# Kernel optimization log

Hardware: AMD Instinct MI355X
Metric: run time of the kernel (lower is better)

The kernel has to match this reference:

```python
import jax, jax.numpy as jnp
import numpy as np

B, V, K, D, E, NE = 32, 512, 16, 128, 32, 8192


def setup_inputs() -> dict:
    key = jax.random.key(0)
    ks = jax.random.split(key, 12)
    s = 0.05
    return {
        "vertex_features": jax.random.normal(ks[0], (B, V, D), jnp.float32),
        "atom_adj": jax.random.randint(ks[1], (B * V * K,), 0, B * V),
        "bond_adj": jax.random.randint(ks[2], (B * V * K,), 0, B * NE),
        "h0": jax.random.normal(ks[3], (B, V, D), jnp.float32),
        "lamda": jnp.full((1,), 0.5, jnp.float32),
        "alpha": jnp.full((1,), 0.1, jnp.float32),
        "l": 1,
        "edge_initial": jax.random.normal(ks[4], (B, NE, E), jnp.float32),
        "vertex_mask": jnp.ones((B, V), jnp.float32),
        "nbs_mask": jax.random.uniform(ks[5], (B, V, K), jnp.float32),
        # label_U1: (D+E) -> D ; label_U2: 2D -> D ; feature_updating: D -> D (variant=False)
        "W1": jax.random.normal(ks[6], (D, D + E), jnp.float32) * s,
        "b1": jax.random.normal(ks[7], (D,), jnp.float32) * s,
        "W2": jax.random.normal(ks[8], (D, 2 * D), jnp.float32) * s,
        "b2": jax.random.normal(ks[9], (D,), jnp.float32) * s,
        "W3": jax.random.normal(ks[10], (D, D), jnp.float32) * s,
        "b3": jax.random.normal(ks[11], (D,), jnp.float32) * s,
    }


def reference(vertex_features, atom_adj, bond_adj, h0, lamda, alpha, l,
              edge_initial, vertex_mask, nbs_mask, W1, b1, W2, b2, W3, b3):
    b, v = vertex_mask.shape
    k = nbs_mask.shape[2]
    d = vertex_features.shape[-1]
    e = edge_initial.shape[-1]
    # gather neighbor vertex and edge features (flat index, torch.index_select semantics)
    vn = vertex_features.reshape(-1, d)[atom_adj].reshape(b, v, k, d)
    en = edge_initial.reshape(-1, e)[bond_adj].reshape(b, v, k, e)
    l_neighbor = jnp.concatenate([vn, en], axis=-1)            # [b,v,k,d+e]
    nl = jax.nn.gelu(l_neighbor @ W1.T + b1, approximate=False)  # exact GELU like torch F.gelu
    nl = jnp.sum(nl * nbs_mask[..., None], axis=-2)            # masked sum over neighbors -> [b,v,d]
    hi = jnp.concatenate([nl, vertex_features], axis=-1) @ W2.T + b2
    theta = jnp.log(lamda / l + 1.0)                           # broadcast scalar (shape [1])
    support = (1.0 - alpha) * hi + alpha * h0                  # variant=False: r == support
    out = theta * (support @ W3.T + b3) + (1.0 - theta) * support
    out = out + vertex_features                                # residual=True
    return out
```

## Files before the change

### kernel.cpp

```cpp
#include <hip/hip_runtime.h>
#include <hip/hip_bf16.h>
#include <math.h>

#define NLSTR 136
#define ASTR  168

typedef __bf16 bf16x8 __attribute__((ext_vector_type(8)));
typedef float f32x4 __attribute__((ext_vector_type(4)));
typedef float f32x16 __attribute__((ext_vector_type(16)));
typedef unsigned short ushort8v __attribute__((ext_vector_type(8)));

union FragU { ushort8v u; bf16x8 b; };

static __device__ inline unsigned short f2bf(float f){
  unsigned u = __float_as_uint(f);
  u += 0x7fffu + ((u >> 16) & 1u);
  return (unsigned short)(u >> 16);
}
static __device__ inline float bf2f(unsigned short u){
  return __uint_as_float(((unsigned)u) << 16);
}
static __device__ inline unsigned pk2(float a, float b){
  union { __hip_bfloat162 h; unsigned u; } r;
  r.h = __float22bfloat162_rn(float2{a, b});
  return r.u;
}
static __device__ inline ushort8v pkcvt8(float4 a, float4 b){
  union { unsigned u[4]; ushort8v v; } r;
  r.u[0] = pk2(a.x, a.y); r.u[1] = pk2(a.z, a.w);
  r.u[2] = pk2(b.x, b.y); r.u[3] = pk2(b.z, b.w);
  return r.v;
}

static __device__ inline float gelu_f(float x){
  float u = x * x;
  float p = fmaf(u, 0.07135481283f, 1.5957691216f);
  float t = x * p;
  float e = __builtin_amdgcn_exp2f(t * -1.44269504f);
  return x * __builtin_amdgcn_rcpf(1.0f + e);
}

#define WG_BARRIER() asm volatile("s_waitcnt lgkmcnt(0)\n\ts_barrier" ::: "memory")

__global__ __launch_bounds__(256) void prep_kernel(
    const float* __restrict__ vf, const float* __restrict__ W1,
    const float* __restrict__ W2, const float* __restrict__ W3,
    unsigned short* __restrict__ vfbf, unsigned short* __restrict__ w1f,
    unsigned short* __restrict__ w2f, unsigned short* __restrict__ w3f)
{
  int t = blockIdx.x * 256 + threadIdx.x;
  if (t < 262144){
    const float4* src = (const float4*)vf;
    float4 x = src[t * 2], y = src[t * 2 + 1];
    *(ushort8v*)(vfbf + t * 8) = pkcvt8(x, y);
    return;
  }
  int t2 = t - 262144;
  const float* s;
  unsigned short* d;
  if (t2 < 2560){
    int fragid = t2 >> 6, lane = t2 & 63;
    int nc2 = fragid / 10, kc = fragid % 10, n = lane & 31, h = lane >> 5;
    s = W1 + (nc2 * 32 + n) * 160 + kc * 16 + h * 8;
    d = w1f + t2 * 8;
  } else if (t2 < 6656){
    int t3 = t2 - 2560;
    int fragid = t3 >> 6, lane = t3 & 63;
    int kc = fragid >> 3, nc = fragid & 7, col = lane & 15, quad = lane >> 4;
    s = W2 + (nc * 16 + col) * 256 + kc * 32 + quad * 8;
    d = w2f + t3 * 8;
  } else if (t2 < 8704){
    int t3 = t2 - 6656;
    int fragid = t3 >> 6, lane = t3 & 63;
    int kc = fragid >> 3, nc = fragid & 7, col = lane & 15, quad = lane >> 4;
    s = W3 + (nc * 16 + col) * 128 + kc * 32 + quad * 8;
    d = w3f + t3 * 8;
  } else return;
#pragma unroll
  for (int j = 0; j < 8; j++) d[j] = f2bf(s[j]);
}

__global__ __launch_bounds__(256, 3) void fused_kernel(
    const unsigned short* __restrict__ vfbf,
    const float* __restrict__ vf,
    const int* __restrict__ aadj, const int* __restrict__ badj,
    const float* __restrict__ edge, const float* __restrict__ nbs,
    const float* __restrict__ h0,
    const unsigned short* __restrict__ w1f, const unsigned short* __restrict__ w2f,
    const unsigned short* __restrict__ w3f,
    const float* __restrict__ b1, const float* __restrict__ b2, const float* __restrict__ b3,
    const float* __restrict__ lamda, const float* __restrict__ alpha,
    const int* __restrict__ lval,
    float* __restrict__ out)
{
  __shared__ __align__(16) unsigned short abuf[4][32 * ASTR];
  __shared__ __align__(16) unsigned short nl_lds[16 * NLSTR];
  __shared__ __align__(16) unsigned short sup_lds[16 * NLSTR];
  __shared__ __align__(16) float nbs_lds[256];
  const int wid  = threadIdx.x >> 6;
  const int lane = threadIdx.x & 63;
  const int n32  = lane & 31;
  const int h    = lane >> 5;
  const int col  = lane & 15;
  const int quad = lane >> 4;
  const int v0   = blockIdx.x * 16;

  const int srow = threadIdx.x >> 3;
  const int ssub = threadIdx.x & 7;

  int a_all[8], e_all[8];
  {
    const int base = (v0 + (srow >> 4)) * 16 + (srow & 15);
#pragma unroll
    for (int p = 0; p < 8; p++){
      a_all[p] = aadj[base + 32 * p];
      e_all[p] = badj[base + 32 * p];
    }
  }

  ushort8v sv[4][2]; float4 se[4];
#pragma unroll
  for (int q = 0; q < 4; q++){
    const ushort8v* vs = (const ushort8v*)(vfbf + (size_t)a_all[q] * 128 + ssub * 16);
    sv[q][0] = vs[0]; sv[q][1] = vs[1];
    se[q] = *(const float4*)(edge + (size_t)e_all[q] * 32 + ssub * 4);
  }

  nbs_lds[threadIdx.x] = nbs[v0 * 16 + threadIdx.x];

  FragU bw[10];
#pragma unroll
  for (int kc = 0; kc < 10; kc++)
    bw[kc].u = *(const ushort8v*)(w1f + ((wid * 10 + kc) * 64 + lane) * 8);

  const float bb1 = b1[wid * 32 + n32];

#pragma unroll
  for (int q = 0; q < 4; q++){
    unsigned short* dst = abuf[q] + srow * ASTR + ssub * 16;
    *(ushort8v*)dst = sv[q][0]; *(ushort8v*)(dst + 8) = sv[q][1];
    unsigned* ed = (unsigned*)(abuf[q] + srow * ASTR + 128 + ssub * 4);
    ed[0] = pk2(se[q].x, se[q].y); ed[1] = pk2(se[q].z, se[q].w);
  }
  WG_BARRIER();

#pragma unroll
  for (int q = 0; q < 4; q++){
    const ushort8v* vs = (const ushort8v*)(vfbf + (size_t)a_all[q + 4] * 128 + ssub * 16);
    sv[q][0] = vs[0]; sv[q][1] = vs[1];
    se[q] = *(const float4*)(edge + (size_t)e_all[q + 4] * 32 + ssub * 4);
  }

  const float4* nbsl = (const float4*)nbs_lds;

#pragma unroll
  for (int p = 0; p < 4; p++){
    const float4 mAlo = nbsl[8 * p + h],     mAhi = nbsl[8 * p + 2 + h];
    const float4 mBlo = nbsl[8 * p + 4 + h], mBhi = nbsl[8 * p + 6 + h];
    const unsigned short* ab = abuf[p] + n32 * ASTR + h * 8;
    f32x16 accA = {}, accB = {};
#pragma unroll
    for (int kc = 0; kc < 10; kc += 2){
      FragU fa0, fa1;
      fa0.u = *(const ushort8v*)(ab + kc * 16);
      fa1.u = *(const ushort8v*)(ab + (kc + 1) * 16);
      accA = __builtin_amdgcn_mfma_f32_32x32x16_bf16(fa0.b, bw[kc].b,     accA, 0, 0, 0);
      accB = __builtin_amdgcn_mfma_f32_32x32x16_bf16(fa1.b, bw[kc + 1].b, accB, 0, 0, 0);
    }
    f32x16 acc = accA + accB;
    float sA = gelu_f(acc[0] + bb1) * mAlo.x + gelu_f(acc[1] + bb1) * mAlo.y
             + gelu_f(acc[2] + bb1) * mAlo.z + gelu_f(acc[3] + bb1) * mAlo.w
             + gelu_f(acc[4] + bb1) * mAhi.x + gelu_f(acc[5] + bb1) * mAhi.y
             + gelu_f(acc[6] + bb1) * mAhi.z + gelu_f(acc[7] + bb1) * mAhi.w;
    float sB = gelu_f(acc[8] + bb1) * mBlo.x + gelu_f(acc[9] + bb1) * mBlo.y
             + gelu_f(acc[10] + bb1) * mBlo.z + gelu_f(acc[11] + bb1) * mBlo.w
             + gelu_f(acc[12] + bb1) * mBhi.x + gelu_f(acc[13] + bb1) * mBhi.y
             + gelu_f(acc[14] + bb1) * mBhi.z + gelu_f(acc[15] + bb1) * mBhi.w;
    sA += __shfl_xor(sA, 32, 64);
    sB += __shfl_xor(sB, 32, 64);
    if (h == 0) nl_lds[(2 * p)     * NLSTR + wid * 32 + n32] = f2bf(sA);
    else        nl_lds[(2 * p + 1) * NLSTR + wid * 32 + n32] = f2bf(sB);
  }
  WG_BARRIER();

#pragma unroll
  for (int q = 0; q < 4; q++){
    unsigned short* dst = abuf[q] + srow * ASTR + ssub * 16;
    *(ushort8v*)dst = sv[q][0]; *(ushort8v*)(dst + 8) = sv[q][1];
    unsigned* ed = (unsigned*)(abuf[q] + srow * ASTR + 128 + ssub * 4);
    ed[0] = pk2(se[q].x, se[q].y); ed[1] = pk2(se[q].z, se[q].w);
  }
  WG_BARRIER();

#pragma unroll
  for (int p = 0; p < 4; p++){
    const int pp = p + 4;
    const float4 mAlo = nbsl[8 * pp + h],     mAhi = nbsl[8 * pp + 2 + h];
    const float4 mBlo = nbsl[8 * pp + 4 + h], mBhi = nbsl[8 * pp + 6 + h];
    const unsigned short* ab = abuf[p] + n32 * ASTR + h * 8;
    f32x16 accA = {}, accB = {};
#pragma unroll
    for (int kc = 0; kc < 10; kc += 2){
      FragU fa0, fa1;
      fa0.u = *(const ushort8v*)(ab + kc * 16);
      fa1.u = *(const ushort8v*)(ab + (kc + 1) * 16);
      accA = __builtin_amdgcn_mfma_f32_32x32x16_bf16(fa0.b, bw[kc].b,     accA, 0, 0, 0);
      accB = __builtin_amdgcn_mfma_f32_32x32x16_bf16(fa1.b, bw[kc + 1].b, accB, 0, 0, 0);
    }
    f32x16 acc = accA + accB;
    float sA = gelu_f(acc[0] + bb1) * mAlo.x + gelu_f(acc[1] + bb1) * mAlo.y
             + gelu_f(acc[2] + bb1) * mAlo.z + gelu_f(acc[3] + bb1) * mAlo.w
             + gelu_f(acc[4] + bb1) * mAhi.x + gelu_f(acc[5] + bb1) * mAhi.y
             + gelu_f(acc[6] + bb1) * mAhi.z + gelu_f(acc[7] + bb1) * mAhi.w;
    float sB = gelu_f(acc[8] + bb1) * mBlo.x + gelu_f(acc[9] + bb1) * mBlo.y
             + gelu_f(acc[10] + bb1) * mBlo.z + gelu_f(acc[11] + bb1) * mBlo.w
             + gelu_f(acc[12] + bb1) * mBhi.x + gelu_f(acc[13] + bb1) * mBhi.y
             + gelu_f(acc[14] + bb1) * mBhi.z + gelu_f(acc[15] + bb1) * mBhi.w;
    sA += __shfl_xor(sA, 32, 64);
    sB += __shfl_xor(sB, 32, 64);
    if (h == 0) nl_lds[(2 * pp)     * NLSTR + wid * 32 + n32] = f2bf(sA);
    else        nl_lds[(2 * pp + 1) * NLSTR + wid * 32 + n32] = f2bf(sB);
  }
  __syncthreads();

  const int nc0 = 2 * wid;
  const float th = logf(lamda[0] / (float)lval[0] + 1.0f);
  const float al = alpha[0];

  float h0v[2][4];
#pragma unroll
  for (int pq = 0; pq < 2; pq++){
    const int d = (nc0 + pq) * 16 + col;
#pragma unroll
    for (int r = 0; r < 4; r++)
      h0v[pq][r] = h0[(v0 + quad * 4 + r) * 128 + d];
  }

  f32x4 acc2[2] = {};
#pragma unroll
  for (int kc = 0; kc < 8; kc++){
    FragU a;
    if (kc < 4) a.u = *(const ushort8v*)(nl_lds + col * NLSTR + kc * 32 + quad * 8);
    else        a.u = *(const ushort8v*)(vfbf + (size_t)(v0 + col) * 128 + (kc - 4) * 32 + quad * 8);
#pragma unroll
    for (int pq = 0; pq < 2; pq++){
      FragU bf_;
      bf_.u = *(const ushort8v*)(w2f + ((kc * 8 + nc0 + pq) * 64 + lane) * 8);
      acc2[pq] = __builtin_amdgcn_mfma_f32_16x16x32_bf16(a.b, bf_.b, acc2[pq], 0, 0, 0);
    }
  }

  float sup[2][4];
#pragma unroll
  for (int pq = 0; pq < 2; pq++){
    const int d = (nc0 + pq) * 16 + col;
    const float bb = b2[d];
#pragma unroll
    for (int r = 0; r < 4; r++){
      float hi = acc2[pq][r] + bb;
      float s = (1.f - al) * hi + al * h0v[pq][r];
      sup[pq][r] = s;
      sup_lds[(quad * 4 + r) * NLSTR + d] = f2bf(s);
    }
  }
  __syncthreads();

  float rv[2][4];
#pragma unroll
  for (int pq = 0; pq < 2; pq++){
    const int d = (nc0 + pq) * 16 + col;
#pragma unroll
    for (int r = 0; r < 4; r++)
      rv[pq][r] = vf[(size_t)(v0 + quad * 4 + r) * 128 + d];
  }

  f32x4 acc3[2] = {};
#pragma unroll
  for (int kc = 0; kc < 4; kc++){
    FragU a;
    a.u = *(const ushort8v*)(sup_lds + col * NLSTR + kc * 32 + quad * 8);
#pragma unroll
    for (int pq = 0; pq < 2; pq++){
      FragU bf_;
      bf_.u = *(const ushort8v*)(w3f + ((kc * 8 + nc0 + pq) * 64 + lane) * 8);
      acc3[pq] = __builtin_amdgcn_mfma_f32_16x16x32_bf16(a.b, bf_.b, acc3[pq], 0, 0, 0);
    }
  }

#pragma unroll
  for (int pq = 0; pq < 2; pq++){
    const int d = (nc0 + pq) * 16 + col;
    const float bb = b3[d];
#pragma unroll
    for (int r = 0; r < 4; r++){
      const int vtx = v0 + quad * 4 + r;
      out[vtx * 128 + d] = th * (acc3[pq][r] + bb) + (1.f - th) * sup[pq][r] + rv[pq][r];
    }
  }
}

extern "C" void kernel_launch(void* const* d_in, const int* in_sizes, int n_in,
                              void* d_out, int out_size, void* d_ws, size_t ws_size,
                              hipStream_t stream)
{
  const float* vfp  = (const float*)d_in[0];
  const int*   aadj = (const int*)d_in[1];
  const int*   badj = (const int*)d_in[2];
  const float* h0   = (const float*)d_in[3];
  const float* lam  = (const float*)d_in[4];
  const float* alp  = (const float*)d_in[5];
  const int*   lv   = (const int*)d_in[6];
  const float* edge = (const float*)d_in[7];
  const float* nbs  = (const float*)d_in[9];
  const float* W1   = (const float*)d_in[10];
  const float* b1   = (const float*)d_in[11];
  const float* W2   = (const float*)d_in[12];
  const float* b2   = (const float*)d_in[13];
  const float* W3   = (const float*)d_in[14];
  const float* b3   = (const float*)d_in[15];
  float* out = (float*)d_out;

  unsigned short* w1f  = (unsigned short*)d_ws;
  unsigned short* w2f  = w1f + 20480;
  unsigned short* w3f  = w2f + 32768;
  unsigned short* vfbf = w3f + 16384;

  prep_kernel<<<1058, 256, 0, stream>>>(vfp, W1, W2, W3, vfbf, w1f, w2f, w3f);
  fused_kernel<<<1024, 256, 0, stream>>>(vfbf, vfp, aadj, badj, edge, nbs, h0,
                                         w1f, w2f, w3f, b1, b2, b3, lam, alp, lv, out);
}
```

Measured before the change: 136.0 us.

## Prewarm L2 with bulk loads, fold bias into MFMA init, simplify GELU

Each block issues coalesced dummy loads over a slice of the bf16 vertex features and edge features, so later random gathers are more likely to hit L2; an empty asm keeps the loads from being removed. The bias is now used as the initial MFMA accumulator, and the two interleaved accumulator chains become one serial chain. GELU's constants are folded so it needs one fewer multiply, and the masked sums use fma. The prewarm costs extra registers and bandwidth, and the single MFMA chain may expose more dependency latency.

Result: no change. 136.2 us (+0.2%).

```diff
diff --git a/kernel.cpp b/kernel.cpp
--- a/kernel.cpp
+++ b/kernel.cpp
@@ -16,9 +16,6 @@
   unsigned u = __float_as_uint(f);
   u += 0x7fffu + ((u >> 16) & 1u);
   return (unsigned short)(u >> 16);
-}
-static __device__ inline float bf2f(unsigned short u){
-  return __uint_as_float(((unsigned)u) << 16);
 }
 static __device__ inline unsigned pk2(float a, float b){
   union { __hip_bfloat162 h; unsigned u; } r;
@@ -34,9 +31,8 @@
 
 static __device__ inline float gelu_f(float x){
   float u = x * x;
-  float p = fmaf(u, 0.07135481283f, 1.5957691216f);
-  float t = x * p;
-  float e = __builtin_amdgcn_exp2f(t * -1.44269504f);
+  float p = fmaf(u, -0.1029434273f, -2.3022084765f);
+  float e = __builtin_amdgcn_exp2f(x * p);
   return x * __builtin_amdgcn_rcpf(1.0f + e);
 }
 
@@ -108,6 +104,19 @@
   const int srow = threadIdx.x >> 3;
   const int ssub = threadIdx.x & 7;
 
+  float4 wu[10];
+  {
+    const float4* vsrc = (const float4*)vfbf;
+    const int vb = (blockIdx.x >> 3) * 2048 + threadIdx.x;
+#pragma unroll
+    for (int i = 0; i < 8; i++) wu[i] = vsrc[vb + i * 256];
+    const float4* esrc = (const float4*)edge;
+    const int eb = (blockIdx.x >> 3) * 512 + threadIdx.x;
+    wu[8] = esrc[eb]; wu[9] = esrc[eb + 256];
+  }
+
+  nbs_lds[threadIdx.x] = nbs[v0 * 16 + threadIdx.x];
+
   int a_all[8], e_all[8];
   {
     const int base = (v0 + (srow >> 4)) * 16 + (srow & 15);
@@ -117,6 +126,10 @@
       e_all[p] = badj[base + 32 * p];
     }
   }
+
+#pragma unroll
+  for (int i = 0; i < 10; i++)
+    asm volatile("" :: "v"(wu[i].x), "v"(wu[i].y), "v"(wu[i].z), "v"(wu[i].w));
 
   ushort8v sv[4][2]; float4 se[4];
 #pragma unroll
@@ -125,8 +138,6 @@
     sv[q][0] = vs[0]; sv[q][1] = vs[1];
     se[q] = *(const float4*)(edge + (size_t)e_all[q] * 32 + ssub * 4);
   }
-
-  nbs_lds[threadIdx.x] = nbs[v0 * 16 + threadIdx.x];
 
   FragU bw[10];
 #pragma unroll
@@ -158,24 +169,23 @@
     const float4 mAlo = nbsl[8 * p + h],     mAhi = nbsl[8 * p + 2 + h];
     const float4 mBlo = nbsl[8 * p + 4 + h], mBhi = nbsl[8 * p + 6 + h];
     const unsigned short* ab = abuf[p] + n32 * ASTR + h * 8;
-    f32x16 accA = {}, accB = {};
-#pragma unroll
-    for (int kc = 0; kc < 10; kc += 2){
-      FragU fa0, fa1;
-      fa0.u = *(const ushort8v*)(ab + kc * 16);
-      fa1.u = *(const ushort8v*)(ab + (kc + 1) * 16);
-      accA = __builtin_amdgcn_mfma_f32_32x32x16_bf16(fa0.b, bw[kc].b,     accA, 0, 0, 0);
-      accB = __builtin_amdgcn_mfma_f32_32x32x16_bf16(fa1.b, bw[kc + 1].b, accB, 0, 0, 0);
-    }
-    f32x16 acc = accA + accB;
-    float sA = gelu_f(acc[0] + bb1) * mAlo.x + gelu_f(acc[1] + bb1) * mAlo.y
-             + gelu_f(acc[2] + bb1) * mAlo.z + gelu_f(acc[3] + bb1) * mAlo.w
-             + gelu_f(acc[4] + bb1) * mAhi.x + gelu_f(acc[5] + bb1) * mAhi.y
-             + gelu_f(acc[6] + bb1) * mAhi.z + gelu_f(acc[7] + bb1) * mAhi.w;
-    float sB = gelu_f(acc[8] + bb1) * mBlo.x + gelu_f(acc[9] + bb1) * mBlo.y
-             + gelu_f(acc[10] + bb1) * mBlo.z + gelu_f(acc[11] + bb1) * mBlo.w
-             + gelu_f(acc[12] + bb1) * mBhi.x + gelu_f(acc[13] + bb1) * mBhi.y
-             + gelu_f(acc[14] + bb1) * mBhi.z + gelu_f(acc[15] + bb1) * mBhi.w;
+    f32x16 acc;
+#pragma unroll
+    for (int j = 0; j < 16; j++) acc[j] = bb1;
+#pragma unroll
+    for (int kc = 0; kc < 10; kc++){
+      FragU fa;
+      fa.u = *(const ushort8v*)(ab + kc * 16);
+      acc = __builtin_amdgcn_mfma_f32_32x32x16_bf16(fa.b, bw[kc].b, acc, 0, 0, 0);
+    }
+    float sA = fmaf(gelu_f(acc[0]),  mAlo.x, gelu_f(acc[1])  * mAlo.y)
+             + fmaf(gelu_f(acc[2]),  mAlo.z, gelu_f(acc[3])  * mAlo.w)
+             + fmaf(gelu_f(acc[4]),  mAhi.x, gelu_f(acc[5])  * mAhi.y)
+             + fmaf(gelu_f(acc[6]),  mAhi.z, gelu_f(acc[7])  * mAhi.w);
+    float sB = fmaf(gelu_f(acc[8]),  mBlo.x, gelu_f(acc[9])  * mBlo.y)
+             + fmaf(gelu_f(acc[10]), mBlo.z, gelu_f(acc[11]) * mBlo.w)
+             + fmaf(gelu_f(acc[12]), mBhi.x, gelu_f(acc[13]) * mBhi.y)
+             + fmaf(gelu_f(acc[14]), mBhi.z, gelu_f(acc[15]) * mBhi.w);
     sA += __shfl_xor(sA, 32, 64);
     sB += __shfl_xor(sB, 32, 64);
     if (h == 0) nl_lds[(2 * p)     * NLSTR + wid * 32 + n32] = f2bf(sA);
@@ -198,24 +208,23 @@
     const float4 mAlo = nbsl[8 * pp + h],     mAhi = nbsl[8 * pp + 2 + h];
     const float4 mBlo = nbsl[8 * pp + 4 + h], mBhi = nbsl[8 * pp + 6 + h];
     const unsigned short* ab = abuf[p] + n32 * ASTR + h * 8;
-    f32x16 accA = {}, accB = {};
-#pragma unroll
-    for (int kc = 0; kc < 10; kc += 2){
-      FragU fa0, fa1;
-      fa0.u = *(const ushort8v*)(ab + kc * 16);
-      fa1.u = *(const ushort8v*)(ab + (kc + 1) * 16);
-      accA = __builtin_amdgcn_mfma_f32_32x32x16_bf16(fa0.b, bw[kc].b,     accA, 0, 0, 0);
-      accB = __builtin_amdgcn_mfma_f32_32x32x16_bf16(fa1.b, bw[kc + 1].b, accB, 0, 0, 0);
-    }
-    f32x16 acc = accA + accB;
-    float sA = gelu_f(acc[0] + bb1) * mAlo.x + gelu_f(acc[1] + bb1) * mAlo.y
-             + gelu_f(acc[2] + bb1) * mAlo.z + gelu_f(acc[3] + bb1) * mAlo.w
-             + gelu_f(acc[4] + bb1) * mAhi.x + gelu_f(acc[5] + bb1) * mAhi.y
-             + gelu_f(acc[6] + bb1) * mAhi.z + gelu_f(acc[7] + bb1) * mAhi.w;
-    float sB = gelu_f(acc[8] + bb1) * mBlo.x + gelu_f(acc[9] + bb1) * mBlo.y
-             + gelu_f(acc[10] + bb1) * mBlo.z + gelu_f(acc[11] + bb1) * mBlo.w
-             + gelu_f(acc[12] + bb1) * mBhi.x + gelu_f(acc[13] + bb1) * mBhi.y
-             + gelu_f(acc[14] + bb1) * mBhi.z + gelu_f(acc[15] + bb1) * mBhi.w;
+    f32x16 acc;
+#pragma unroll
+    for (int j = 0; j < 16; j++) acc[j] = bb1;
+#pragma unroll
+    for (int kc = 0; kc < 10; kc++){
+      FragU fa;
+      fa.u = *(const ushort8v*)(ab + kc * 16);
+      acc = __builtin_amdgcn_mfma_f32_32x32x16_bf16(fa.b, bw[kc].b, acc, 0, 0, 0);
+    }
+    float sA = fmaf(gelu_f(acc[0]),  mAlo.x, gelu_f(acc[1])  * mAlo.y)
+             + fmaf(gelu_f(acc[2]),  mAlo.z, gelu_f(acc[3])  * mAlo.w)
+             + fmaf(gelu_f(acc[4]),  mAhi.x, gelu_f(acc[5])  * mAhi.y)
+             + fmaf(gelu_f(acc[6]),  mAhi.z, gelu_f(acc[7])  * mAhi.w);
+    float sB = fmaf(gelu_f(acc[8]),  mBlo.x, gelu_f(acc[9])  * mBlo.y)
+             + fmaf(gelu_f(acc[10]), mBlo.z, gelu_f(acc[11]) * mBlo.w)
+             + fmaf(gelu_f(acc[12]), mBhi.x, gelu_f(acc[13]) * mBhi.y)
+             + fmaf(gelu_f(acc[14]), mBhi.z, gelu_f(acc[15]) * mBhi.w);
     sA += __shfl_xor(sA, 32, 64);
     sB += __shfl_xor(sB, 32, 64);
     if (h == 0) nl_lds[(2 * pp)     * NLSTR + wid * 32 + n32] = f2bf(sA);
```
